# Kernel tuning notes

Hardware: AMD Instinct MI355X
Metric: run time of the kernel (lower is better)

The kernel has to match this reference:

```python
import jax, jax.numpy as jnp
import numpy as np
from itertools import product

# Static config
B, H, W, C = 16, 64, 64, 256
WIN = 8            # window size (square)
SHIFT = 4          # cyclic shift
NH = 8             # heads
HD = C // NH       # head dim
N = WIN * WIN      # tokens per window
HIDDEN = 1024


def _rel_pos_index():
    coords = np.stack(np.meshgrid(np.arange(WIN), np.arange(WIN), indexing='ij'))  # (2,w,w)
    flat = coords.reshape(2, -1)                                   # (2,N)
    rel = flat[:, :, None] - flat[:, None, :]                      # (2,N,N)
    rel = rel.transpose(1, 2, 0).astype(np.int64)
    rel[..., 0] += WIN - 1
    rel[..., 1] += WIN - 1
    rel[..., 0] *= 2 * WIN - 1
    return rel.sum(-1)                                             # (N,N)


def _shift_mask():
    # additive mask (nW, N, N) with -100 across shift boundaries (generate_mask)
    img = np.zeros((H, W), dtype=np.float32)
    slices = [(slice(0, -WIN), slice(-WIN, -SHIFT), slice(-SHIFT, None))] * 2
    cnt = 0
    for sx, sy in product(*slices):
        img[sx, sy] = cnt
        cnt += 1
    mw = img.reshape(H // WIN, WIN, W // WIN, WIN).transpose(0, 2, 1, 3).reshape(-1, N)  # (nW,N)
    diff = mw[:, None, :] - mw[:, :, None]
    return np.where(diff != 0, -100.0, 0.0).astype(np.float32)     # (nW,N,N)


REL_IDX = jnp.asarray(_rel_pos_index())
MASK = jnp.asarray(_shift_mask())


def _layernorm(x, scale, bias, eps=1e-5):
    mu = jnp.mean(x, axis=-1, keepdims=True)
    var = jnp.mean(jnp.square(x - mu), axis=-1, keepdims=True)
    return (x - mu) * jax.lax.rsqrt(var + eps) * scale + bias


def setup_inputs() -> dict:
    key = jax.random.key(0)
    ks = jax.random.split(key, 8)
    s = lambda fan_in: 1.0 / np.sqrt(fan_in)
    return {
        'x': jax.random.normal(ks[0], (B, H, W, C), jnp.float32),
        'ln1_scale': jnp.ones((C,), jnp.float32),
        'ln1_bias': jnp.zeros((C,), jnp.float32),
        'qkv_w': jax.random.normal(ks[1], (3 * C, C), jnp.float32) * s(C),
        'qkv_b': jnp.zeros((3 * C,), jnp.float32),
        'proj_w': jax.random.normal(ks[2], (C, C), jnp.float32) * s(C),
        'proj_b': jnp.zeros((C,), jnp.float32),
        'rel_bias': jax.random.normal(ks[3], ((2 * WIN - 1) ** 2, NH), jnp.float32) * 0.02,
        'ln2_scale': jnp.ones((C,), jnp.float32),
        'ln2_bias': jnp.zeros((C,), jnp.float32),
        'mlp_w1': jax.random.normal(ks[4], (HIDDEN, C), jnp.float32) * s(C),
        'mlp_b1': jnp.zeros((HIDDEN,), jnp.float32),
        'mlp_w2': jax.random.normal(ks[5], (C, HIDDEN), jnp.float32) * s(HIDDEN),
        'mlp_b2': jnp.zeros((C,), jnp.float32),
    }


def reference(x, ln1_scale, ln1_bias, qkv_w, qkv_b, proj_w, proj_b, rel_bias,
              ln2_scale, ln2_bias, mlp_w1, mlp_b1, mlp_w2, mlp_b2):
    nWh, nWw = H // WIN, W // WIN
    nW = nWh * nWw

    shortcut = x
    h = _layernorm(x, ln1_scale, ln1_bias)
    # cyclic shift
    h = jnp.roll(h, shift=(-SHIFT, -SHIFT), axis=(1, 2))
    # window partition -> (B*nW, N, C)
    h = h.reshape(B, nWh, WIN, nWw, WIN, C).transpose(0, 1, 3, 2, 4, 5).reshape(B * nW, N, C)

    # qkv
    qkv = h @ qkv_w.T + qkv_b                                # (B*nW, N, 3C)
    qkv = qkv.reshape(B * nW, N, 3, NH, HD)
    q, k, v = qkv[:, :, 0], qkv[:, :, 1], qkv[:, :, 2]       # (B*nW, N, NH, HD)

    scale = 1.0 / np.sqrt(HD)
    attn = jnp.einsum('bnhd,bmhd->bhnm', q * scale, k)       # (B*nW, NH, N, N)
    attn = attn + rel_bias[REL_IDX].transpose(2, 0, 1)[None]  # rel-pos bias (NH,N,N)
    attn = attn.reshape(B, nW, NH, N, N) + MASK[None, :, None]
    attn = jax.nn.softmax(attn.reshape(B * nW, NH, N, N), axis=-1)

    out = jnp.einsum('bhnm,bmhd->bnhd', attn, v).reshape(B * nW, N, C)
    out = out @ proj_w.T + proj_b

    # window reverse + reverse shift
    out = out.reshape(B, nWh, nWw, WIN, WIN, C).transpose(0, 1, 3, 2, 4, 5).reshape(B, H, W, C)
    out = jnp.roll(out, shift=(SHIFT, SHIFT), axis=(1, 2))

    x = shortcut + out
    # MLP
    h2 = _layernorm(x, ln2_scale, ln2_bias)
    h2 = jax.nn.gelu(h2 @ mlp_w1.T + mlp_b1, approximate=False) @ mlp_w2.T + mlp_b2
    return x + h2
```

## Files before the change

kernel.cpp:

```cpp
#include <hip/hip_runtime.h>
#include <hip/hip_bf16.h>
#include <math.h>

#define AS1 __attribute__((address_space(1)))
#define AS3 __attribute__((address_space(3)))

typedef __bf16  bf16x8 __attribute__((ext_vector_type(8)));
typedef float   f32x4  __attribute__((ext_vector_type(4)));
typedef __hip_bfloat16 bf16;

__device__ __forceinline__ void gload_lds16(const void* g, void* l) {
  __builtin_amdgcn_global_load_lds((const AS1 void*)g, (AS3 void*)l, 16, 0, 0);
}

__global__ __launch_bounds__(256) void k_conv_weights(
    const float* __restrict__ qkvw, const float* __restrict__ projw,
    const float* __restrict__ w1, const float* __restrict__ w2,
    bf16* __restrict__ dst)
{
  int i = blockIdx.x * 256 + threadIdx.x;
  float v;
  if (i < 196608)       v = qkvw[i];
  else if (i < 262144)  v = projw[i - 196608];
  else if (i < 524288)  v = w1[i - 262144];
  else                  v = w2[i - 524288];
  dst[i] = __float2bfloat16(v);
}

__global__ __launch_bounds__(256) void k_build_btab(
    const float* __restrict__ rel_bias, float* __restrict__ btab)
{
  int i = blockIdx.x * 256 + threadIdx.x;
  int h = i >> 12, r = i & 4095, n = r >> 6, m = r & 63;
  int idx = ((n >> 3) - (m >> 3) + 7) * 15 + ((n & 7) - (m & 7) + 7);
  btab[i] = rel_bias[idx * 8 + h];
}

__global__ __launch_bounds__(256) void k_ln1_window(
    const float* __restrict__ x, const float* __restrict__ sc,
    const float* __restrict__ bi, bf16* __restrict__ hout)
{
  int t = blockIdx.x * 4 + (threadIdx.x >> 6);
  int lane = threadIdx.x & 63;
  int win = t >> 6, nn = t & 63;
  int b = win >> 6, ww = win & 63;
  int ry = ((ww >> 3) << 3) + (nn >> 3);
  int rx = ((ww & 7) << 3) + (nn & 7);
  int sy = (ry + 4) & 63, sx = (rx + 4) & 63;
  const float* src = x + ((size_t)(((b << 6) + sy) << 6) + sx) * 256;
  f32x4 v = *(const f32x4*)(src + lane * 4);
  float s = v[0] + v[1] + v[2] + v[3];
  #pragma unroll
  for (int o = 1; o < 64; o <<= 1) s += __shfl_xor(s, o);
  float mu = s * (1.0f / 256.0f);
  float d0 = v[0]-mu, d1 = v[1]-mu, d2 = v[2]-mu, d3 = v[3]-mu;
  float q = d0*d0 + d1*d1 + d2*d2 + d3*d3;
  #pragma unroll
  for (int o = 1; o < 64; o <<= 1) q += __shfl_xor(q, o);
  float rstd = rsqrtf(q * (1.0f / 256.0f) + 1e-5f);
  int c = lane * 4;
  union { bf16 h[4]; uint2 u; } pk;
  pk.h[0] = __float2bfloat16(d0 * rstd * sc[c+0] + bi[c+0]);
  pk.h[1] = __float2bfloat16(d1 * rstd * sc[c+1] + bi[c+1]);
  pk.h[2] = __float2bfloat16(d2 * rstd * sc[c+2] + bi[c+2]);
  pk.h[3] = __float2bfloat16(d3 * rstd * sc[c+3] + bi[c+3]);
  *(uint2*)(hout + (size_t)t * 256 + c) = pk.u;
}

template<int EPI>
__global__ __launch_bounds__(256, 2) void k_pipe_ar(
    const bf16* __restrict__ A, const bf16* __restrict__ Bw,
    const float* __restrict__ bias,
    float* __restrict__ Cf, bf16* __restrict__ Cb,
    const float* __restrict__ resid,
    const float* __restrict__ ln2s, const float* __restrict__ ln2b,
    bf16* __restrict__ ln2out, int N)
{
  __shared__ __align__(16) char lds[65536 + 10240];

  const int tid = threadIdx.x;
  const int wid = tid >> 6;
  const int lane = tid & 63;
  const int l15 = lane & 15, lh = lane >> 4;
  const int rowBase = blockIdx.x * 128 + wid * 32;
  const int NC = N >> 5;
  char* scr = lds + 65536 + wid * 2560;

  auto stage = [&](int c) {
    char* dst = lds + (c & 3) * 16384;
    const char* srcB = (const char*)Bw + (size_t)c * 32 * 512;
    #pragma unroll
    for (int i = 0; i < 4; ++i) {
      int off = (i * 256 + tid) * 16;
      int r = off >> 9, cb = off & 511;
      int csw = cb ^ ((r & 7) << 4);
      gload_lds16(srcB + (size_t)r * 512 + csw, dst + off);
    }
  };

  bf16x8 af[2][8];
  {
    const bf16* a0 = A + (size_t)(rowBase + l15) * 256 + lh * 8;
    #pragma unroll
    for (int kk = 0; kk < 8; ++kk) {
      af[0][kk] = *(const bf16x8*)(a0 + kk * 32);
      af[1][kk] = *(const bf16x8*)(a0 + 4096 + kk * 32);
    }
  }

  auto remap = [&](int row) -> size_t {
    int win = row >> 6, nn = row & 63;
    int b = win >> 6, ww = win & 63;
    int ry = ((ww >> 3) << 3) + (nn >> 3);
    int rx = ((ww & 7) << 3) + (nn & 7);
    int fy = (ry + 4) & 63, fx = (rx + 4) & 63;
    return ((size_t)(((b << 6) + fy) << 6) + fx) * 256;
  };
  size_t ra0 = 0, ra1 = 0;
  size_t rbA, rbB;
  if (EPI == 2) {
    ra0 = remap(rowBase + l15);
    ra1 = remap(rowBase + 16 + l15);
    rbA = remap(rowBase + (lane >> 2));
    rbB = remap(rowBase + 16 + (lane >> 2));
  } else {
    rbA = (size_t)(rowBase + (lane >> 2)) * N;
    rbB = rbA + (size_t)16 * N;
  }

  const int cl = lh * 4;
  f32x4 bc0 = *(const f32x4*)(bias + cl);
  f32x4 bc1 = *(const f32x4*)(bias + cl + 16);
  f32x4 rc00, rc10, rc01, rc11;
  if (EPI == 2) {
    rc00 = *(const f32x4*)(resid + ra0 + cl);
    rc10 = *(const f32x4*)(resid + ra1 + cl);
    rc01 = *(const f32x4*)(resid + ra0 + cl + 16);
    rc11 = *(const f32x4*)(resid + ra1 + cl + 16);
  }
  stage(0); stage(1); stage(2);
  asm volatile("s_waitcnt vmcnt(8)" ::: "memory");
  __builtin_amdgcn_sched_barrier(0);

  float s0 = 0.f, q0 = 0.f, s1 = 0.f, q1 = 0.f;

  for (int c = 0; c < NC; ++c) {
    __builtin_amdgcn_s_barrier();
    __builtin_amdgcn_sched_barrier(0);

    f32x4 bn0, bn1, rn00, rn10, rn01, rn11;
    if (c + 1 < NC) {
      const int ncl = (c + 1) * 32 + cl;
      bn0 = *(const f32x4*)(bias + ncl);
      bn1 = *(const f32x4*)(bias + ncl + 16);
      if (EPI == 2) {
        rn00 = *(const f32x4*)(resid + ra0 + ncl);
        rn10 = *(const f32x4*)(resid + ra1 + ncl);
        rn01 = *(const f32x4*)(resid + ra0 + ncl + 16);
        rn11 = *(const f32x4*)(resid + ra1 + ncl + 16);
      }
    }
    if (c + 3 < NC) stage(c + 3);

    const char* buf = lds + (c & 3) * 16384;
    const int xr = (l15 & 7) << 4;
    const int base0 = l15 * 512;
    f32x4 a00 = (f32x4){0.f,0.f,0.f,0.f};
    f32x4 a10 = (f32x4){0.f,0.f,0.f,0.f};
    f32x4 a01 = (f32x4){0.f,0.f,0.f,0.f};
    f32x4 a11 = (f32x4){0.f,0.f,0.f,0.f};
    #pragma unroll
    for (int kk = 0; kk < 8; ++kk) {
      const int ko = (kk * 64 + lh * 16) ^ xr;
      bf16x8 b0 = *(const bf16x8*)(buf + base0 + ko);
      bf16x8 b1 = *(const bf16x8*)(buf + base0 + 8192 + ko);
      a00 = __builtin_amdgcn_mfma_f32_16x16x32_bf16(b0, af[0][kk], a00, 0, 0, 0);
      a10 = __builtin_amdgcn_mfma_f32_16x16x32_bf16(b0, af[1][kk], a10, 0, 0, 0);
      a01 = __builtin_amdgcn_mfma_f32_16x16x32_bf16(b1, af[0][kk], a01, 0, 0, 0);
      a11 = __builtin_amdgcn_mfma_f32_16x16x32_bf16(b1, af[1][kk], a11, 0, 0, 0);
    }

    const int cbs = c * 32 + (lane & 3) * 8;
    if (EPI == 0) {
      union { bf16 h[4]; uint2 u; } p00, p01, p10, p11;
      #pragma unroll
      for (int j = 0; j < 4; ++j) {
        p00.h[j] = __float2bfloat16(a00[j] + bc0[j]);
        p01.h[j] = __float2bfloat16(a01[j] + bc1[j]);
        p10.h[j] = __float2bfloat16(a10[j] + bc0[j]);
        p11.h[j] = __float2bfloat16(a11[j] + bc1[j]);
      }
      *(uint2*)(scr + l15 * 80 + lh * 8)            = p00.u;
      *(uint2*)(scr + l15 * 80 + 32 + lh * 8)       = p01.u;
      *(uint2*)(scr + (16 + l15) * 80 + lh * 8)     = p10.u;
      *(uint2*)(scr + (16 + l15) * 80 + 32 + lh * 8)= p11.u;
      uint4 r0 = *(const uint4*)(scr + (lane >> 2) * 80 + (lane & 3) * 16);
      uint4 r1 = *(const uint4*)(scr + (16 + (lane >> 2)) * 80 + (lane & 3) * 16);
      *(uint4*)(Cb + rbA + cbs) = r0;
      *(uint4*)(Cb + rbB + cbs) = r1;
    } else {
      const int colb0 = c * 32 + cl, colb1 = colb0 + 16;
      f32x4 o00, o10, o01, o11;
      #pragma unroll
      for (int j = 0; j < 4; ++j) {
        o00[j] = a00[j] + bc0[j] + rc00[j];
        o10[j] = a10[j] + bc0[j] + rc10[j];
        o01[j] = a01[j] + bc1[j] + rc01[j];
        o11[j] = a11[j] + bc1[j] + rc11[j];
      }
      *(f32x4*)(Cf + ra0 + colb0) = o00;
      *(f32x4*)(Cf + ra1 + colb0) = o10;
      *(f32x4*)(Cf + ra0 + colb1) = o01;
      *(f32x4*)(Cf + ra1 + colb1) = o11;
      #pragma unroll
      for (int j = 0; j < 4; ++j) {
        s0 += o00[j] + o01[j];  q0 += o00[j]*o00[j] + o01[j]*o01[j];
        s1 += o10[j] + o11[j];  q1 += o10[j]*o10[j] + o11[j]*o11[j];
      }
    }

    if (c + 1 < NC) {
      bc0 = bn0; bc1 = bn1;
      if (EPI == 2) { rc00 = rn00; rc10 = rn10; rc01 = rn01; rc11 = rn11; }
    }

    if (c + 1 < NC) {
      if (EPI == 2) {
        if (c == 0)            { asm volatile("s_waitcnt vmcnt(18)" ::: "memory"); }
        else if (c + 3 < NC)   { asm volatile("s_waitcnt vmcnt(28)" ::: "memory"); }
        else                   { asm volatile("s_waitcnt vmcnt(6)"  ::: "memory"); }
      } else {
        if (c == 0)            { asm volatile("s_waitcnt vmcnt(12)" ::: "memory"); }
        else if (c + 3 < NC)   { asm volatile("s_waitcnt vmcnt(16)" ::: "memory"); }
        else                   { asm volatile("s_waitcnt vmcnt(6)"  ::: "memory"); }
      }
      __builtin_amdgcn_sched_barrier(0);
    }
  }

  if (EPI == 2) {
    s0 += __shfl_xor(s0, 16); s0 += __shfl_xor(s0, 32);
    q0 += __shfl_xor(q0, 16); q0 += __shfl_xor(q0, 32);
    s1 += __shfl_xor(s1, 16); s1 += __shfl_xor(s1, 32);
    q1 += __shfl_xor(q1, 16); q1 += __shfl_xor(q1, 32);
    float mu0 = s0 * (1.0f / 256.0f);
    float rs0 = rsqrtf(q0 * (1.0f / 256.0f) - mu0 * mu0 + 1e-5f);
    float mu1 = s1 * (1.0f / 256.0f);
    float rs1 = rsqrtf(q1 * (1.0f / 256.0f) - mu1 * mu1 + 1e-5f);
    for (int c = 0; c < NC; ++c) {
      const int cb0 = c * 32 + cl, cb1 = cb0 + 16;
      f32x4 v00 = *(const f32x4*)(Cf + ra0 + cb0);
      f32x4 v01 = *(const f32x4*)(Cf + ra0 + cb1);
      f32x4 v10 = *(const f32x4*)(Cf + ra1 + cb0);
      f32x4 v11 = *(const f32x4*)(Cf + ra1 + cb1);
      f32x4 sa = *(const f32x4*)(ln2s + cb0);
      f32x4 sb = *(const f32x4*)(ln2s + cb1);
      f32x4 ba = *(const f32x4*)(ln2b + cb0);
      f32x4 bb = *(const f32x4*)(ln2b + cb1);
      union { bf16 h[4]; uint2 u; } p00, p01, p10, p11;
      #pragma unroll
      for (int j = 0; j < 4; ++j) {
        p00.h[j] = __float2bfloat16((v00[j] - mu0) * rs0 * sa[j] + ba[j]);
        p01.h[j] = __float2bfloat16((v01[j] - mu0) * rs0 * sb[j] + bb[j]);
        p10.h[j] = __float2bfloat16((v10[j] - mu1) * rs1 * sa[j] + ba[j]);
        p11.h[j] = __float2bfloat16((v11[j] - mu1) * rs1 * sb[j] + bb[j]);
      }
      *(uint2*)(scr + l15 * 80 + lh * 8)             = p00.u;
      *(uint2*)(scr + l15 * 80 + 32 + lh * 8)        = p01.u;
      *(uint2*)(scr + (16 + l15) * 80 + lh * 8)      = p10.u;
      *(uint2*)(scr + (16 + l15) * 80 + 32 + lh * 8) = p11.u;
      uint4 r0 = *(const uint4*)(scr + (lane >> 2) * 80 + (lane & 3) * 16);
      uint4 r1 = *(const uint4*)(scr + (16 + (lane >> 2)) * 80 + (lane & 3) * 16);
      const int cbs = c * 32 + (lane & 3) * 8;
      *(uint4*)(ln2out + rbA + cbs) = r0;
      *(uint4*)(ln2out + rbB + cbs) = r1;
    }
  }
}

__global__ __launch_bounds__(512, 2) void k_mlp(
    const bf16* __restrict__ A, const bf16* __restrict__ W1,
    const float* __restrict__ B1, const bf16* __restrict__ W2,
    const float* __restrict__ B2, float* __restrict__ X1)
{
  __shared__ __align__(16) char lds[122880];

  const int tid = threadIdx.x;
  const int wid = tid >> 6;
  const int lane = tid & 63;
  const int l15 = lane & 15, lh = lane >> 4;
  const int rowBase = blockIdx.x * 256 + wid * 32;
  char* scr   = lds + 98304 + wid * 2560;
  char* b1lds = lds + 118784;

  auto stage_w1 = [&](int c) {
    char* slot = lds + (c % 3) * 32768;
    const char* srcW1 = (const char*)W1 + (size_t)c * 32 * 512;
    #pragma unroll
    for (int i = 0; i < 2; ++i) {
      int off = (i * 512 + tid) * 16;
      int r = off >> 9, cb = off & 511;
      int csw = cb ^ ((r & 7) << 4);
      gload_lds16(srcW1 + (size_t)r * 512 + csw, slot + off);
    }
  };
  auto stage_w2 = [&](int c) {
    char* dst = lds + ((c + 1) % 3) * 32768 + 16384;
    #pragma unroll
    for (int i = 0; i < 2; ++i) {
      int off = (i * 512 + tid) * 16;
      int ch = off >> 12, row = (off >> 4) & 255;
      gload_lds16((const char*)W2 + (size_t)row * 2048 + (size_t)c * 64 + ch * 16,
                  dst + off);
    }
  };

  if (tid < 256) gload_lds16((const char*)B1 + tid * 16, b1lds + tid * 16);
  bf16x8 af[2][8];
  {
    const bf16* a0 = A + (size_t)(rowBase + l15) * 256 + lh * 8;
    #pragma unroll
    for (int kk = 0; kk < 8; ++kk) {
      af[0][kk] = *(const bf16x8*)(a0 + kk * 32);
      af[1][kk] = *(const bf16x8*)(a0 + 4096 + kk * 32);
    }
  }
  stage_w1(0);
  stage_w1(1);
  stage_w2(0);
  asm volatile("s_waitcnt vmcnt(4)" ::: "memory");
  __builtin_amdgcn_sched_barrier(0);

  f32x4 acc2[2][16];
  #pragma unroll
  for (int m = 0; m < 2; ++m)
    #pragma unroll
    for (int n = 0; n < 16; ++n) acc2[m][n] = (f32x4){0.f,0.f,0.f,0.f};
  bf16x8 actfA = {}, actfB = {};

  for (int c = 0; c < 32; ++c) {
    __builtin_amdgcn_s_barrier();
    __builtin_amdgcn_sched_barrier(0);

    if (c + 2 < 32) stage_w1(c + 2);
    if (c + 1 < 32) stage_w2(c + 1);

    const char* slot  = lds + (c % 3) * 32768;
    const char* w2buf = slot + 16384;
    const int xr = (l15 & 7) << 4;
    const int base0 = l15 * 512;
    const int w2k = lh * 4096;
    f32x4 a00 = (f32x4){0.f,0.f,0.f,0.f};
    f32x4 a10 = (f32x4){0.f,0.f,0.f,0.f};
    f32x4 a01 = (f32x4){0.f,0.f,0.f,0.f};
    f32x4 a11 = (f32x4){0.f,0.f,0.f,0.f};
    if (c > 0) {
      #pragma unroll
      for (int kk = 0; kk < 8; ++kk) {
        const int ko = (kk * 64 + lh * 16) ^ xr;
        bf16x8 b0 = *(const bf16x8*)(slot + base0 + ko);
        bf16x8 b1 = *(const bf16x8*)(slot + base0 + 8192 + ko);
        a00 = __builtin_amdgcn_mfma_f32_16x16x32_bf16(b0, af[0][kk], a00, 0, 0, 0);
        a10 = __builtin_amdgcn_mfma_f32_16x16x32_bf16(b0, af[1][kk], a10, 0, 0, 0);
        a01 = __builtin_amdgcn_mfma_f32_16x16x32_bf16(b1, af[0][kk], a01, 0, 0, 0);
        a11 = __builtin_amdgcn_mfma_f32_16x16x32_bf16(b1, af[1][kk], a11, 0, 0, 0);
        bf16x8 w0 = *(const bf16x8*)(w2buf + w2k + ((2*kk)   * 16 + l15) * 16);
        bf16x8 w1f= *(const bf16x8*)(w2buf + w2k + ((2*kk+1) * 16 + l15) * 16);
        acc2[0][2*kk]   = __builtin_amdgcn_mfma_f32_16x16x32_bf16(w0,  actfA, acc2[0][2*kk],   0, 0, 0);
        acc2[1][2*kk]   = __builtin_amdgcn_mfma_f32_16x16x32_bf16(w0,  actfB, acc2[1][2*kk],   0, 0, 0);
        acc2[0][2*kk+1] = __builtin_amdgcn_mfma_f32_16x16x32_bf16(w1f, actfA, acc2[0][2*kk+1], 0, 0, 0);
        acc2[1][2*kk+1] = __builtin_amdgcn_mfma_f32_16x16x32_bf16(w1f, actfB, acc2[1][2*kk+1], 0, 0, 0);
      }
    } else {
      #pragma unroll
      for (int kk = 0; kk < 8; ++kk) {
        const int ko = (kk * 64 + lh * 16) ^ xr;
        bf16x8 b0 = *(const bf16x8*)(slot + base0 + ko);
        bf16x8 b1 = *(const bf16x8*)(slot + base0 + 8192 + ko);
        a00 = __builtin_amdgcn_mfma_f32_16x16x32_bf16(b0, af[0][kk], a00, 0, 0, 0);
        a10 = __builtin_amdgcn_mfma_f32_16x16x32_bf16(b0, af[1][kk], a10, 0, 0, 0);
        a01 = __builtin_amdgcn_mfma_f32_16x16x32_bf16(b1, af[0][kk], a01, 0, 0, 0);
        a11 = __builtin_amdgcn_mfma_f32_16x16x32_bf16(b1, af[1][kk], a11, 0, 0, 0);
      }
    }

    f32x4 bv0 = *(const f32x4*)(b1lds + c * 128 + lh * 16);
    f32x4 bv1 = *(const f32x4*)(b1lds + c * 128 + 64 + lh * 16);
    auto gelu = [](float v) -> bf16 {
      float w = fmaf(v * v, 0.1029434f, 2.3022083f);
      float e = __builtin_amdgcn_exp2f(-v * w);
      return __float2bfloat16(v * __builtin_amdgcn_rcpf(1.0f + e));
    };
    union { bf16 h[4]; uint2 u; } p00, p01, p10, p11;
    #pragma unroll
    for (int j = 0; j < 4; ++j) {
      p00.h[j] = gelu(a00[j] + bv0[j]);
      p01.h[j] = gelu(a01[j] + bv1[j]);
      p10.h[j] = gelu(a10[j] + bv0[j]);
      p11.h[j] = gelu(a11[j] + bv1[j]);
    }
    *(uint2*)(scr + l15 * 80 + lh * 8)             = p00.u;
    *(uint2*)(scr + l15 * 80 + 32 + lh * 8)        = p01.u;
    *(uint2*)(scr + (16 + l15) * 80 + lh * 8)      = p10.u;
    *(uint2*)(scr + (16 + l15) * 80 + 32 + lh * 8) = p11.u;
    actfA = *(const bf16x8*)(scr + l15 * 80 + lh * 16);
    actfB = *(const bf16x8*)(scr + (16 + l15) * 80 + lh * 16);

    if (c <= 29)      { asm volatile("s_waitcnt vmcnt(4)" ::: "memory"); }
    else if (c == 30) { asm volatile("s_waitcnt vmcnt(2)" ::: "memory"); }
    else              { asm volatile("s_waitcnt vmcnt(0)" ::: "memory"); }
    __builtin_amdgcn_sched_barrier(0);
  }

  __builtin_amdgcn_s_barrier();
  {
    const char* w2buf = lds + 2 * 32768 + 16384;
    const int w2k = lh * 4096;
    #pragma unroll
    for (int n = 0; n < 16; ++n) {
      bf16x8 wf = *(const bf16x8*)(w2buf + w2k + (n * 16 + l15) * 16);
      acc2[0][n] = __builtin_amdgcn_mfma_f32_16x16x32_bf16(wf, actfA, acc2[0][n], 0, 0, 0);
      acc2[1][n] = __builtin_amdgcn_mfma_f32_16x16x32_bf16(wf, actfB, acc2[1][n], 0, 0, 0);
    }
  }

  #pragma unroll
  for (int m = 0; m < 2; ++m) {
    size_t rowAddr = (size_t)(rowBase + m * 16 + l15) * 256;
    #pragma unroll
    for (int n = 0; n < 16; ++n) {
      const int colb = n * 16 + lh * 4;
      const f32x4 b4 = *(const f32x4*)(B2 + colb);
      f32x4* p = (f32x4*)(X1 + rowAddr + colb);
      f32x4 cc = *p;
      #pragma unroll
      for (int j = 0; j < 4; ++j) cc[j] += acc2[m][n][j] + b4[j];
      *p = cc;
    }
  }
}

__global__ __launch_bounds__(256) void k_attn(
    const bf16* __restrict__ qkv, const float* __restrict__ btab,
    bf16* __restrict__ outp)
{
  __shared__ __align__(16) char smem[71680];
  float* sb = (float*)smem;
  const int tid = threadIdx.x, wid = tid >> 6, lane = tid & 63;
  const int l15 = lane & 15, lh = lane >> 4;
  const int h = blockIdx.x >> 8;
  const int win = ((blockIdx.x & 255) << 2) + wid;
  const int tb = win << 6;
  char* plw = smem + 16384 + wid * 9216;
  char* vtw = smem + 16384 + 36864 + wid * 4608;

  for (int i = tid; i < 4096; i += 256) sb[i] = btab[(h << 12) + i];
  __syncthreads();

  bf16x8 qf[4], kf[4];
  #pragma unroll
  for (int m = 0; m < 4; ++m) {
    size_t base = (size_t)(tb + m * 16 + l15) * 768 + h * 32 + lh * 8;
    qf[m] = *(const bf16x8*)(qkv + base);
    kf[m] = *(const bf16x8*)(qkv + base + 256);
  }
  f32x4 s[4][4];
  #pragma unroll
  for (int i = 0; i < 4; ++i)
    #pragma unroll
    for (int j = 0; j < 4; ++j) {
      s[i][j] = (f32x4){0.f,0.f,0.f,0.f};
      s[i][j] = __builtin_amdgcn_mfma_f32_16x16x32_bf16(qf[i], kf[j], s[i][j], 0, 0, 0);
    }

  {
    const bf16* vrow = qkv + (size_t)(tb + lane) * 768 + 512 + h * 32;
    union { uint4 u; bf16 h8[8]; } v0, v1, v2, v3;
    v0.u = *(const uint4*)(vrow);
    v1.u = *(const uint4*)(vrow + 8);
    v2.u = *(const uint4*)(vrow + 16);
    v3.u = *(const uint4*)(vrow + 24);
    #pragma unroll
    for (int j = 0; j < 8; ++j) {
      *(bf16*)(vtw + (j)      * 144 + lane * 2) = v0.h8[j];
      *(bf16*)(vtw + (8 + j)  * 144 + lane * 2) = v1.h8[j];
      *(bf16*)(vtw + (16 + j) * 144 + lane * 2) = v2.h8[j];
      *(bf16*)(vtw + (24 + j) * 144 + lane * 2) = v3.h8[j];
    }
  }

  int ww = win & 63, wi = ww >> 3, wj = ww & 7;
  int labm[4];
  #pragma unroll
  for (int jf = 0; jf < 4; ++jf) {
    int m = jf * 16 + l15;
    int yy = wi * 8 + (m >> 3), xx = wj * 8 + (m & 7);
    labm[jf] = (yy < 56 ? 0 : (yy < 60 ? 1 : 2)) * 3 + (xx < 56 ? 0 : (xx < 60 ? 1 : 2));
  }
  float rsum[4][4];
  const float scale = 0.17677669529663687f;
  #pragma unroll
  for (int i = 0; i < 4; ++i) {
    #pragma unroll
    for (int j = 0; j < 4; ++j) {
      int n = i * 16 + lh * 4 + j;
      int yy = wi * 8 + (n >> 3), xx = wj * 8 + (n & 7);
      int labn = (yy < 56 ? 0 : (yy < 60 ? 1 : 2)) * 3 + (xx < 56 ? 0 : (xx < 60 ? 1 : 2));
      float vals[4]; float mx = -1e30f;
      #pragma unroll
      for (int jf = 0; jf < 4; ++jf) {
        int m = jf * 16 + l15;
        float v = s[i][jf][j] * scale + sb[(n << 6) + m];
        if (labn != labm[jf]) v -= 100.0f;
        vals[jf] = v; mx = fmaxf(mx, v);
      }
      #pragma unroll
      for (int o = 1; o < 16; o <<= 1) mx = fmaxf(mx, __shfl_xor(mx, o));
      float sum = 0.0f;
      #pragma unroll
      for (int jf = 0; jf < 4; ++jf) {
        float e = __expf(vals[jf] - mx);
        sum += e;
        *(bf16*)(plw + n * 144 + (jf * 16 + l15) * 2) = __float2bfloat16(e);
      }
      #pragma unroll
      for (int o = 1; o < 16; o <<= 1) sum += __shfl_xor(sum, o);
      rsum[i][j] = sum;
    }
  }
  __syncthreads();

  f32x4 o[4][2];
  #pragma unroll
  for (int i = 0; i < 4; ++i) { o[i][0] = (f32x4){0.f,0.f,0.f,0.f}; o[i][1] = (f32x4){0.f,0.f,0.f,0.f}; }
  #pragma unroll
  for (int kk = 0; kk < 2; ++kk) {
    bf16x8 pf[4], vf[2];
    #pragma unroll
    for (int i = 0; i < 4; ++i)
      pf[i] = *(const bf16x8*)(plw + (i * 16 + l15) * 144 + kk * 64 + lh * 16);
    #pragma unroll
    for (int df = 0; df < 2; ++df)
      vf[df] = *(const bf16x8*)(vtw + (df * 16 + l15) * 144 + kk * 64 + lh * 16);
    #pragma unroll
    for (int i = 0; i < 4; ++i)
      #pragma unroll
      for (int df = 0; df < 2; ++df)
        o[i][df] = __builtin_amdgcn_mfma_f32_16x16x32_bf16(pf[i], vf[df], o[i][df], 0, 0, 0);
  }
  #pragma unroll
  for (int i = 0; i < 4; ++i)
    #pragma unroll
    for (int df = 0; df < 2; ++df)
      #pragma unroll
      for (int j = 0; j < 4; ++j) {
        int n = i * 16 + lh * 4 + j;
        int d = df * 16 + l15;
        float v = o[i][df][j] / rsum[i][j];
        outp[(size_t)(tb + n) * 256 + h * 32 + d] = __float2bfloat16(v);
      }
}

extern "C" void kernel_launch(void* const* d_in, const int* in_sizes, int n_in,
                              void* d_out, int out_size, void* d_ws, size_t ws_size,
                              hipStream_t stream) {
  (void)in_sizes; (void)n_in; (void)out_size; (void)ws_size;
  const float* x      = (const float*)d_in[0];
  const float* ln1_s  = (const float*)d_in[1];
  const float* ln1_b  = (const float*)d_in[2];
  const float* qkv_w  = (const float*)d_in[3];
  const float* qkv_b  = (const float*)d_in[4];
  const float* proj_w = (const float*)d_in[5];
  const float* proj_b = (const float*)d_in[6];
  const float* rel_b  = (const float*)d_in[7];
  const float* ln2_s  = (const float*)d_in[8];
  const float* ln2_b  = (const float*)d_in[9];
  const float* w1     = (const float*)d_in[10];
  const float* b1     = (const float*)d_in[11];
  const float* w2     = (const float*)d_in[12];
  const float* b2     = (const float*)d_in[13];

  char* ws = (char*)d_ws;
  bf16*  wqkv  = (bf16*)(ws + 0);
  bf16*  wproj = wqkv + 196608;
  bf16*  wm1   = wqkv + 262144;
  bf16*  wm2   = wqkv + 524288;
  float* btab  = (float*)(ws + 1572864);
  bf16*  hbuf  = (bf16*)(ws + 2097152);
  bf16*  qkvb  = (bf16*)(ws + 35651584);
  bf16*  attnb = (bf16*)(ws + 136314880);
  bf16*  ln2buf = hbuf;
  float* x1    = (float*)d_out;

  k_conv_weights<<<3072, 256, 0, stream>>>(qkv_w, proj_w, w1, w2, wqkv);
  k_build_btab<<<128, 256, 0, stream>>>(rel_b, btab);
  k_ln1_window<<<16384, 256, 0, stream>>>(x, ln1_s, ln1_b, hbuf);
  k_pipe_ar<0><<<512, 256, 0, stream>>>(hbuf, wqkv, qkv_b, nullptr, qkvb, nullptr,
                                        nullptr, nullptr, nullptr, 768);
  k_attn<<<2048, 256, 0, stream>>>(qkvb, btab, attnb);
  k_pipe_ar<2><<<512, 256, 0, stream>>>(attnb, wproj, proj_b, x1, nullptr, x,
                                        ln2_s, ln2_b, ln2buf, 256);
  k_mlp<<<256, 512, 0, stream>>>(ln2buf, wm1, b1, wm2, b2, x1);
}
```

Before: 269.6 us.

## Split templated GEMM into qkv/proj kernels with 64-row-per-wave tiles

Replaces the templated k_pipe_ar with two specialised kernels, k_qkv and k_proj. Each wave now handles 64 rows instead of 32, so every LDS-staged weight fragment feeds twice as many MFMAs and the grid halves to 256 blocks. The weight pipeline drops from four stages to three so the larger per-wave scratch still fits in shared memory, and residual loads are issued inside the loop rather than prefetched a chunk ahead. The cost is higher register pressure from a 4x8 A-fragment array, fewer blocks to spread across CUs, and hand-tuned vmcnt waits that must match the new load counts.

```diff
diff --git a/kernel.cpp b/kernel.cpp
--- a/kernel.cpp
+++ b/kernel.cpp
@@ -11,6 +11,15 @@
 
 __device__ __forceinline__ void gload_lds16(const void* g, void* l) {
   __builtin_amdgcn_global_load_lds((const AS1 void*)g, (AS3 void*)l, 16, 0, 0);
+}
+
+__device__ __forceinline__ size_t win_remap(int row) {
+  int w2 = row >> 6, nn2 = row & 63;
+  int b2 = w2 >> 6, ww3 = w2 & 63;
+  int ry = ((ww3 >> 3) << 3) + (nn2 >> 3);
+  int rx = ((ww3 & 7) << 3) + (nn2 & 7);
+  int fy = (ry + 4) & 63, fx = (rx + 4) & 63;
+  return ((size_t)(((b2 << 6) + fy) << 6) + fx) * 256;
 }
 
 __global__ __launch_bounds__(256) void k_conv_weights(
@@ -67,27 +76,21 @@
   *(uint2*)(hout + (size_t)t * 256 + c) = pk.u;
 }
 
-template<int EPI>
-__global__ __launch_bounds__(256, 2) void k_pipe_ar(
+__global__ __launch_bounds__(256, 2) void k_qkv(
     const bf16* __restrict__ A, const bf16* __restrict__ Bw,
-    const float* __restrict__ bias,
-    float* __restrict__ Cf, bf16* __restrict__ Cb,
-    const float* __restrict__ resid,
-    const float* __restrict__ ln2s, const float* __restrict__ ln2b,
-    bf16* __restrict__ ln2out, int N)
+    const float* __restrict__ bias, bf16* __restrict__ Cb)
 {
-  __shared__ __align__(16) char lds[65536 + 10240];
-
+  __shared__ __align__(16) char lds[69632];
   const int tid = threadIdx.x;
   const int wid = tid >> 6;
   const int lane = tid & 63;
   const int l15 = lane & 15, lh = lane >> 4;
-  const int rowBase = blockIdx.x * 128 + wid * 32;
-  const int NC = N >> 5;
-  char* scr = lds + 65536 + wid * 2560;
+  const int rowBase = blockIdx.x * 256 + wid * 64;
+  char* scr = lds + 49152 + wid * 5120;
+  const int NC = 24;
 
   auto stage = [&](int c) {
-    char* dst = lds + (c & 3) * 16384;
+    char* dst = lds + (c % 3) * 16384;
     const char* srcB = (const char*)Bw + (size_t)c * 32 * 512;
     #pragma unroll
     for (int i = 0; i < 4; ++i) {
@@ -98,182 +101,229 @@
     }
   };
 
-  bf16x8 af[2][8];
-  {
-    const bf16* a0 = A + (size_t)(rowBase + l15) * 256 + lh * 8;
-    #pragma unroll
-    for (int kk = 0; kk < 8; ++kk) {
-      af[0][kk] = *(const bf16x8*)(a0 + kk * 32);
-      af[1][kk] = *(const bf16x8*)(a0 + 4096 + kk * 32);
-    }
-  }
-
-  auto remap = [&](int row) -> size_t {
-    int win = row >> 6, nn = row & 63;
-    int b = win >> 6, ww = win & 63;
-    int ry = ((ww >> 3) << 3) + (nn >> 3);
-    int rx = ((ww & 7) << 3) + (nn & 7);
-    int fy = (ry + 4) & 63, fx = (rx + 4) & 63;
-    return ((size_t)(((b << 6) + fy) << 6) + fx) * 256;
-  };
-  size_t ra0 = 0, ra1 = 0;
-  size_t rbA, rbB;
-  if (EPI == 2) {
-    ra0 = remap(rowBase + l15);
-    ra1 = remap(rowBase + 16 + l15);
-    rbA = remap(rowBase + (lane >> 2));
-    rbB = remap(rowBase + 16 + (lane >> 2));
-  } else {
-    rbA = (size_t)(rowBase + (lane >> 2)) * N;
-    rbB = rbA + (size_t)16 * N;
-  }
-
-  const int cl = lh * 4;
-  f32x4 bc0 = *(const f32x4*)(bias + cl);
-  f32x4 bc1 = *(const f32x4*)(bias + cl + 16);
-  f32x4 rc00, rc10, rc01, rc11;
-  if (EPI == 2) {
-    rc00 = *(const f32x4*)(resid + ra0 + cl);
-    rc10 = *(const f32x4*)(resid + ra1 + cl);
-    rc01 = *(const f32x4*)(resid + ra0 + cl + 16);
-    rc11 = *(const f32x4*)(resid + ra1 + cl + 16);
-  }
-  stage(0); stage(1); stage(2);
-  asm volatile("s_waitcnt vmcnt(8)" ::: "memory");
+  f32x4 bc0 = *(const f32x4*)(bias + lh * 4);
+  f32x4 bc1 = *(const f32x4*)(bias + 16 + lh * 4);
+
+  bf16x8 af[4][8];
+  #pragma unroll
+  for (int m = 0; m < 4; ++m) {
+    const bf16* a0 = A + (size_t)(rowBase + m * 16 + l15) * 256 + lh * 8;
+    #pragma unroll
+    for (int kk = 0; kk < 8; ++kk)
+      af[m][kk] = *(const bf16x8*)(a0 + kk * 32);
+  }
+
+  size_t rb[4];
+  #pragma unroll
+  for (int g = 0; g < 4; ++g)
+    rb[g] = (size_t)(rowBase + g * 16 + (lane >> 2)) * 768;
+
+  stage(0); stage(1);
+  asm volatile("s_waitcnt vmcnt(4)" ::: "memory");
   __builtin_amdgcn_sched_barrier(0);
-
-  float s0 = 0.f, q0 = 0.f, s1 = 0.f, q1 = 0.f;
 
   for (int c = 0; c < NC; ++c) {
     __builtin_amdgcn_s_barrier();
     __builtin_amdgcn_sched_barrier(0);
 
-    f32x4 bn0, bn1, rn00, rn10, rn01, rn11;
+    f32x4 bn0, bn1;
     if (c + 1 < NC) {
-      const int ncl = (c + 1) * 32 + cl;
-      bn0 = *(const f32x4*)(bias + ncl);
-      bn1 = *(const f32x4*)(bias + ncl + 16);
-      if (EPI == 2) {
-        rn00 = *(const f32x4*)(resid + ra0 + ncl);
-        rn10 = *(const f32x4*)(resid + ra1 + ncl);
-        rn01 = *(const f32x4*)(resid + ra0 + ncl + 16);
-        rn11 = *(const f32x4*)(resid + ra1 + ncl + 16);
-      }
-    }
-    if (c + 3 < NC) stage(c + 3);
-
-    const char* buf = lds + (c & 3) * 16384;
-    const int xr = (l15 & 7) << 4;
-    const int base0 = l15 * 512;
-    f32x4 a00 = (f32x4){0.f,0.f,0.f,0.f};
-    f32x4 a10 = (f32x4){0.f,0.f,0.f,0.f};
-    f32x4 a01 = (f32x4){0.f,0.f,0.f,0.f};
-    f32x4 a11 = (f32x4){0.f,0.f,0.f,0.f};
+      bn0 = *(const f32x4*)(bias + (c + 1) * 32 + lh * 4);
+      bn1 = *(const f32x4*)(bias + (c + 1) * 32 + 16 + lh * 4);
+    }
+    if (c + 2 < NC) stage(c + 2);
+
+    const char* buf = lds + (c % 3) * 16384;
+    const int xr0 = (l15 & 7) << 4;
+    f32x4 acc[4][2];
+    #pragma unroll
+    for (int m = 0; m < 4; ++m) {
+      acc[m][0] = (f32x4){0.f,0.f,0.f,0.f};
+      acc[m][1] = (f32x4){0.f,0.f,0.f,0.f};
+    }
     #pragma unroll
     for (int kk = 0; kk < 8; ++kk) {
-      const int ko = (kk * 64 + lh * 16) ^ xr;
-      bf16x8 b0 = *(const bf16x8*)(buf + base0 + ko);
-      bf16x8 b1 = *(const bf16x8*)(buf + base0 + 8192 + ko);
-      a00 = __builtin_amdgcn_mfma_f32_16x16x32_bf16(b0, af[0][kk], a00, 0, 0, 0);
-      a10 = __builtin_amdgcn_mfma_f32_16x16x32_bf16(b0, af[1][kk], a10, 0, 0, 0);
-      a01 = __builtin_amdgcn_mfma_f32_16x16x32_bf16(b1, af[0][kk], a01, 0, 0, 0);
-      a11 = __builtin_amdgcn_mfma_f32_16x16x32_bf16(b1, af[1][kk], a11, 0, 0, 0);
-    }
-
+      const int ko = (kk * 64 + lh * 16) ^ xr0;
+      bf16x8 b0 = *(const bf16x8*)(buf + l15 * 512 + ko);
+      bf16x8 b1 = *(const bf16x8*)(buf + (16 + l15) * 512 + ko);
+      #pragma unroll
+      for (int m = 0; m < 4; ++m) {
+        acc[m][0] = __builtin_amdgcn_mfma_f32_16x16x32_bf16(b0, af[m][kk], acc[m][0], 0, 0, 0);
+        acc[m][1] = __builtin_amdgcn_mfma_f32_16x16x32_bf16(b1, af[m][kk], acc[m][1], 0, 0, 0);
+      }
+    }
+
+    #pragma unroll
+    for (int m = 0; m < 4; ++m) {
+      union { bf16 h[4]; uint2 u; } p0, p1;
+      #pragma unroll
+      for (int j = 0; j < 4; ++j) {
+        p0.h[j] = __float2bfloat16(acc[m][0][j] + bc0[j]);
+        p1.h[j] = __float2bfloat16(acc[m][1][j] + bc1[j]);
+      }
+      *(uint2*)(scr + (m * 16 + l15) * 80 + lh * 8)      = p0.u;
+      *(uint2*)(scr + (m * 16 + l15) * 80 + 32 + lh * 8) = p1.u;
+    }
     const int cbs = c * 32 + (lane & 3) * 8;
-    if (EPI == 0) {
-      union { bf16 h[4]; uint2 u; } p00, p01, p10, p11;
+    #pragma unroll
+    for (int g = 0; g < 4; ++g) {
+      uint4 r = *(const uint4*)(scr + (g * 16 + (lane >> 2)) * 80 + (lane & 3) * 16);
+      *(uint4*)(Cb + rb[g] + cbs) = r;
+    }
+    if (c + 1 < NC) { bc0 = bn0; bc1 = bn1; }
+
+    if (c + 1 < NC) {
+      if (c == 0)          { asm volatile("s_waitcnt vmcnt(10)" ::: "memory"); }
+      else if (c + 2 < NC) { asm volatile("s_waitcnt vmcnt(14)" ::: "memory"); }
+      else                 { asm volatile("s_waitcnt vmcnt(10)" ::: "memory"); }
+      __builtin_amdgcn_sched_barrier(0);
+    }
+  }
+}
+
+__global__ __launch_bounds__(256, 2) void k_proj(
+    const bf16* __restrict__ A, const bf16* __restrict__ Bw,
+    const float* __restrict__ bias, float* __restrict__ Cf,
+    const float* __restrict__ resid, const float* __restrict__ ln2s,
+    const float* __restrict__ ln2b, bf16* __restrict__ ln2out)
+{
+  __shared__ __align__(16) char lds[69632];
+  const int tid = threadIdx.x;
+  const int wid = tid >> 6;
+  const int lane = tid & 63;
+  const int l15 = lane & 15, lh = lane >> 4;
+  const int rowBase = blockIdx.x * 256 + wid * 64;
+  char* scr = lds + 49152 + wid * 5120;
+  const int NC = 8;
+
+  auto stage = [&](int c) {
+    char* dst = lds + (c % 3) * 16384;
+    const char* srcB = (const char*)Bw + (size_t)c * 32 * 512;
+    #pragma unroll
+    for (int i = 0; i < 4; ++i) {
+      int off = (i * 256 + tid) * 16;
+      int r = off >> 9, cb = off & 511;
+      int csw = cb ^ ((r & 7) << 4);
+      gload_lds16(srcB + (size_t)r * 512 + csw, dst + off);
+    }
+  };
+
+  bf16x8 af[4][8];
+  #pragma unroll
+  for (int m = 0; m < 4; ++m) {
+    const bf16* a0 = A + (size_t)(rowBase + m * 16 + l15) * 256 + lh * 8;
+    #pragma unroll
+    for (int kk = 0; kk < 8; ++kk)
+      af[m][kk] = *(const bf16x8*)(a0 + kk * 32);
+  }
+
+  size_t pixA[4], rb[4];
+  #pragma unroll
+  for (int m = 0; m < 4; ++m) {
+    pixA[m] = win_remap(rowBase + m * 16 + l15);
+    rb[m]   = win_remap(rowBase + m * 16 + (lane >> 2));
+  }
+
+  stage(0); stage(1);
+  asm volatile("s_waitcnt vmcnt(4)" ::: "memory");
+  __builtin_amdgcn_sched_barrier(0);
+
+  float s4[4] = {0.f,0.f,0.f,0.f}, q4[4] = {0.f,0.f,0.f,0.f};
+
+  for (int c = 0; c < NC; ++c) {
+    __builtin_amdgcn_s_barrier();
+    __builtin_amdgcn_sched_barrier(0);
+
+    const int cloc0 = c * 32 + lh * 4;
+    const int cloc1 = cloc0 + 16;
+    f32x4 bcc0 = *(const f32x4*)(bias + cloc0);
+    f32x4 bcc1 = *(const f32x4*)(bias + cloc1);
+    f32x4 rr[4][2];
+    #pragma unroll
+    for (int m = 0; m < 4; ++m) {
+      rr[m][0] = *(const f32x4*)(resid + pixA[m] + cloc0);
+      rr[m][1] = *(const f32x4*)(resid + pixA[m] + cloc1);
+    }
+    if (c + 2 < NC) stage(c + 2);
+
+    const char* buf = lds + (c % 3) * 16384;
+    const int xr0 = (l15 & 7) << 4;
+    f32x4 acc[4][2];
+    #pragma unroll
+    for (int m = 0; m < 4; ++m) {
+      acc[m][0] = (f32x4){0.f,0.f,0.f,0.f};
+      acc[m][1] = (f32x4){0.f,0.f,0.f,0.f};
+    }
+    #pragma unroll
+    for (int kk = 0; kk < 8; ++kk) {
+      const int ko = (kk * 64 + lh * 16) ^ xr0;
+      bf16x8 b0 = *(const bf16x8*)(buf + l15 * 512 + ko);
+      bf16x8 b1 = *(const bf16x8*)(buf + (16 + l15) * 512 + ko);
+      #pragma unroll
+      for (int m = 0; m < 4; ++m) {
+        acc[m][0] = __builtin_amdgcn_mfma_f32_16x16x32_bf16(b0, af[m][kk], acc[m][0], 0, 0, 0);
+        acc[m][1] = __builtin_amdgcn_mfma_f32_16x16x32_bf16(b1, af[m][kk], acc[m][1], 0, 0, 0);
+      }
+    }
+
+    #pragma unroll
+    for (int m = 0; m < 4; ++m) {
+      f32x4 o0, o1;
       #pragma unroll
       for (int j = 0; j < 4; ++j) {
-        p00.h[j] = __float2bfloat16(a00[j] + bc0[j]);
-        p01.h[j] = __float2bfloat16(a01[j] + bc1[j]);
-        p10.h[j] = __float2bfloat16(a10[j] + bc0[j]);
-        p11.h[j] = __float2bfloat16(a11[j] + bc1[j]);
-      }
-      *(uint2*)(scr + l15 * 80 + lh * 8)            = p00.u;
-      *(uint2*)(scr + l15 * 80 + 32 + lh * 8)       = p01.u;
-      *(uint2*)(scr + (16 + l15) * 80 + lh * 8)     = p10.u;
-      *(uint2*)(scr + (16 + l15) * 80 + 32 + lh * 8)= p11.u;
-      uint4 r0 = *(const uint4*)(scr + (lane >> 2) * 80 + (lane & 3) * 16);
-      uint4 r1 = *(const uint4*)(scr + (16 + (lane >> 2)) * 80 + (lane & 3) * 16);
-      *(uint4*)(Cb + rbA + cbs) = r0;
-      *(uint4*)(Cb + rbB + cbs) = r1;
-    } else {
-      const int colb0 = c * 32 + cl, colb1 = colb0 + 16;
-      f32x4 o00, o10, o01, o11;
+        o0[j] = acc[m][0][j] + bcc0[j] + rr[m][0][j];
+        o1[j] = acc[m][1][j] + bcc1[j] + rr[m][1][j];
+        s4[m] += o0[j] + o1[j];
+        q4[m] += o0[j]*o0[j] + o1[j]*o1[j];
+      }
+      *(f32x4*)(Cf + pixA[m] + cloc0) = o0;
+      *(f32x4*)(Cf + pixA[m] + cloc1) = o1;
+    }
+
+    if (c + 1 < NC) {
+      if (c == 0)          { asm volatile("s_waitcnt vmcnt(22)" ::: "memory"); }
+      else if (c + 2 < NC) { asm volatile("s_waitcnt vmcnt(30)" ::: "memory"); }
+      else                 { asm volatile("s_waitcnt vmcnt(26)" ::: "memory"); }
+      __builtin_amdgcn_sched_barrier(0);
+    }
+  }
+  asm volatile("s_waitcnt vmcnt(0)" ::: "memory");
+  __builtin_amdgcn_sched_barrier(0);
+
+  float mu[4], rs[4];
+  #pragma unroll
+  for (int m = 0; m < 4; ++m) {
+    float s = s4[m], q = q4[m];
+    s += __shfl_xor(s, 16); s += __shfl_xor(s, 32);
+    q += __shfl_xor(q, 16); q += __shfl_xor(q, 32);
+    mu[m] = s * (1.0f / 256.0f);
+    rs[m] = rsqrtf(q * (1.0f / 256.0f) - mu[m] * mu[m] + 1e-5f);
+  }
+  for (int c = 0; c < NC; ++c) {
+    const int cloc0 = c * 32 + lh * 4;
+    const int cloc1 = cloc0 + 16;
+    f32x4 sa = *(const f32x4*)(ln2s + cloc0);
+    f32x4 sb = *(const f32x4*)(ln2s + cloc1);
+    f32x4 ba = *(const f32x4*)(ln2b + cloc0);
+    f32x4 bb = *(const f32x4*)(ln2b + cloc1);
+    #pragma unroll
+    for (int m = 0; m < 4; ++m) {
+      f32x4 v0 = *(const f32x4*)(Cf + pixA[m] + cloc0);
+      f32x4 v1 = *(const f32x4*)(Cf + pixA[m] + cloc1);
+      union { bf16 h[4]; uint2 u; } p0, p1;
       #pragma unroll
       for (int j = 0; j < 4; ++j) {
-        o00[j] = a00[j] + bc0[j] + rc00[j];
-        o10[j] = a10[j] + bc0[j] + rc10[j];
-        o01[j] = a01[j] + bc1[j] + rc01[j];
-        o11[j] = a11[j] + bc1[j] + rc11[j];
-      }
-      *(f32x4*)(Cf + ra0 + colb0) = o00;
-      *(f32x4*)(Cf + ra1 + colb0) = o10;
-      *(f32x4*)(Cf + ra0 + colb1) = o01;
-      *(f32x4*)(Cf + ra1 + colb1) = o11;
-      #pragma unroll
-      for (int j = 0; j < 4; ++j) {
-        s0 += o00[j] + o01[j];  q0 += o00[j]*o00[j] + o01[j]*o01[j];
-        s1 += o10[j] + o11[j];  q1 += o10[j]*o10[j] + o11[j]*o11[j];
-      }
-    }
-
-    if (c + 1 < NC) {
-      bc0 = bn0; bc1 = bn1;
-      if (EPI == 2) { rc00 = rn00; rc10 = rn10; rc01 = rn01; rc11 = rn11; }
-    }
-
-    if (c + 1 < NC) {
-      if (EPI == 2) {
-        if (c == 0)            { asm volatile("s_waitcnt vmcnt(18)" ::: "memory"); }
-        else if (c + 3 < NC)   { asm volatile("s_waitcnt vmcnt(28)" ::: "memory"); }
-        else                   { asm volatile("s_waitcnt vmcnt(6)"  ::: "memory"); }
-      } else {
-        if (c == 0)            { asm volatile("s_waitcnt vmcnt(12)" ::: "memory"); }
-        else if (c + 3 < NC)   { asm volatile("s_waitcnt vmcnt(16)" ::: "memory"); }
-        else                   { asm volatile("s_waitcnt vmcnt(6)"  ::: "memory"); }
-      }
-      __builtin_amdgcn_sched_barrier(0);
-    }
-  }
-
-  if (EPI == 2) {
-    s0 += __shfl_xor(s0, 16); s0 += __shfl_xor(s0, 32);
-    q0 += __shfl_xor(q0, 16); q0 += __shfl_xor(q0, 32);
-    s1 += __shfl_xor(s1, 16); s1 += __shfl_xor(s1, 32);
-    q1 += __shfl_xor(q1, 16); q1 += __shfl_xor(q1, 32);
-    float mu0 = s0 * (1.0f / 256.0f);
-    float rs0 = rsqrtf(q0 * (1.0f / 256.0f) - mu0 * mu0 + 1e-5f);
-    float mu1 = s1 * (1.0f / 256.0f);
-    float rs1 = rsqrtf(q1 * (1.0f / 256.0f) - mu1 * mu1 + 1e-5f);
-    for (int c = 0; c < NC; ++c) {
-      const int cb0 = c * 32 + cl, cb1 = cb0 + 16;
-      f32x4 v00 = *(const f32x4*)(Cf + ra0 + cb0);
-      f32x4 v01 = *(const f32x4*)(Cf + ra0 + cb1);
-      f32x4 v10 = *(const f32x4*)(Cf + ra1 + cb0);
-      f32x4 v11 = *(const f32x4*)(Cf + ra1 + cb1);
-      f32x4 sa = *(const f32x4*)(ln2s + cb0);
-      f32x4 sb = *(const f32x4*)(ln2s + cb1);
-      f32x4 ba = *(const f32x4*)(ln2b + cb0);
-      f32x4 bb = *(const f32x4*)(ln2b + cb1);
-      union { bf16 h[4]; uint2 u; } p00, p01, p10, p11;
-      #pragma unroll
-      for (int j = 0; j < 4; ++j) {
-        p00.h[j] = __float2bfloat16((v00[j] - mu0) * rs0 * sa[j] + ba[j]);
-        p01.h[j] = __float2bfloat16((v01[j] - mu0) * rs0 * sb[j] + bb[j]);
-        p10.h[j] = __float2bfloat16((v10[j] - mu1) * rs1 * sa[j] + ba[j]);
-        p11.h[j] = __float2bfloat16((v11[j] - mu1) * rs1 * sb[j] + bb[j]);
-      }
-      *(uint2*)(scr + l15 * 80 + lh * 8)             = p00.u;
-      *(uint2*)(scr + l15 * 80 + 32 + lh * 8)        = p01.u;
-      *(uint2*)(scr + (16 + l15) * 80 + lh * 8)      = p10.u;
-      *(uint2*)(scr + (16 + l15) * 80 + 32 + lh * 8) = p11.u;
-      uint4 r0 = *(const uint4*)(scr + (lane >> 2) * 80 + (lane & 3) * 16);
-      uint4 r1 = *(const uint4*)(scr + (16 + (lane >> 2)) * 80 + (lane & 3) * 16);
-      const int cbs = c * 32 + (lane & 3) * 8;
-      *(uint4*)(ln2out + rbA + cbs) = r0;
-      *(uint4*)(ln2out + rbB + cbs) = r1;
+        p0.h[j] = __float2bfloat16((v0[j] - mu[m]) * rs[m] * sa[j] + ba[j]);
+        p1.h[j] = __float2bfloat16((v1[j] - mu[m]) * rs[m] * sb[j] + bb[j]);
+      }
+      *(uint2*)(scr + (m * 16 + l15) * 80 + lh * 8)      = p0.u;
+      *(uint2*)(scr + (m * 16 + l15) * 80 + 32 + lh * 8) = p1.u;
+    }
+    const int cbs = c * 32 + (lane & 3) * 8;
+    #pragma unroll
+    for (int g = 0; g < 4; ++g) {
+      uint4 r = *(const uint4*)(scr + (g * 16 + (lane >> 2)) * 80 + (lane & 3) * 16);
+      *(uint4*)(ln2out + rb[g] + cbs) = r;
     }
   }
 }
@@ -595,10 +645,8 @@
   k_conv_weights<<<3072, 256, 0, stream>>>(qkv_w, proj_w, w1, w2, wqkv);
   k_build_btab<<<128, 256, 0, stream>>>(rel_b, btab);
   k_ln1_window<<<16384, 256, 0, stream>>>(x, ln1_s, ln1_b, hbuf);
-  k_pipe_ar<0><<<512, 256, 0, stream>>>(hbuf, wqkv, qkv_b, nullptr, qkvb, nullptr,
-                                        nullptr, nullptr, nullptr, 768);
+  k_qkv<<<256, 256, 0, stream>>>(hbuf, wqkv, qkv_b, qkvb);
   k_attn<<<2048, 256, 0, stream>>>(qkvb, btab, attnb);
-  k_pipe_ar<2><<<512, 256, 0, stream>>>(attnb, wproj, proj_b, x1, nullptr, x,
-                                        ln2_s, ln2_b, ln2buf, 256);
+  k_proj<<<256, 256, 0, stream>>>(attnb, wproj, proj_b, x1, x, ln2_s, ln2_b, ln2buf);
   k_mlp<<<256, 512, 0, stream>>>(ln2buf, wm1, b1, wm2, b2, x1);
 }
```

Result: slower. 294.7 us (+9.3%).
